# Performance work log

Hardware: AMD Instinct MI355X
Metric: run time of the kernel (lower is better)

Reference implementation:

```python
import jax, jax.numpy as jnp
import numpy as np

N, E, D = 50000, 800000, 128
NEG_SLOPE = 0.01  # torch LeakyReLU default


def _linear_params(key, fan_in, fan_out, bias=True):
    k1, k2 = jax.random.split(key)
    bound = 1.0 / np.sqrt(fan_in)
    W = jax.random.uniform(k1, (fan_in, fan_out), minval=-bound, maxval=bound, dtype=jnp.float32)
    if not bias:
        return W
    b = jax.random.uniform(k2, (fan_out,), minval=-bound, maxval=bound, dtype=jnp.float32)
    return W, b


def setup_inputs() -> dict:
    key = jax.random.key(0)
    ks = jax.random.split(key, 8)
    x = jax.random.normal(ks[0], (N, D), dtype=jnp.float32)
    edge_index = jax.random.randint(ks[1], (2, E), 0, N, dtype=jnp.int64)
    Wk, bk = _linear_params(ks[2], D, D)
    Wq, bq = _linear_params(ks[3], D, D)
    Wv, bv = _linear_params(ks[4], D, D)
    Wskip = _linear_params(ks[5], D, D, bias=False)  # lin_skip has bias=False
    b_conv = jnp.zeros((D,), dtype=jnp.float32)       # ResGatedGraphConv bias param
    Wlin, blin = _linear_params(ks[6], D, D)
    return {"x": x, "edge_index": edge_index, "Wk": Wk, "bk": bk, "Wq": Wq,
            "bq": bq, "Wv": Wv, "bv": bv, "Wskip": Wskip, "b_conv": b_conv,
            "Wlin": Wlin, "blin": blin}


def reference(x, edge_index, Wk, bk, Wq, bq, Wv, bv, Wskip, b_conv, Wlin, blin):
    src, dst = edge_index[0], edge_index[1]  # j -> i
    # dense projections on nodes (cheap), gather to edges (memory-bound)
    k = x @ Wk + bk          # [N, D] key of target
    q = x @ Wq + bq          # [N, D] query of source
    v = x @ Wv + bv          # [N, D] value of source
    gate = jax.nn.relu(k[dst] + q[src])      # act=ReLU() per module
    msg = gate * v[src]                       # [E, D]
    agg = jax.ops.segment_sum(msg, dst, num_segments=x.shape[0])  # scatter-add
    x1 = agg + x @ Wskip + b_conv            # root weight + bias
    x2 = jnp.where(x1 >= 0, x1, NEG_SLOPE * x1)  # LeakyReLU
    return x2 @ Wlin + blin
```

## Files before the change

### kernel.cpp

```cpp
#include <hip/hip_runtime.h>

#define DD 128

typedef __attribute__((ext_vector_type(8))) short bf16x8;
typedef __attribute__((ext_vector_type(4))) float f32x4;

__device__ inline unsigned short f2bf(float f) {
    unsigned int u = __float_as_uint(f);
    u += 0x7FFFu + ((u >> 16) & 1u);
    return (unsigned short)(u >> 16);
}
__device__ inline float bf2f(unsigned short s) {
    return __uint_as_float(((unsigned int)s) << 16);
}

template <typename T> __device__ inline T cvt(float f);
template <> __device__ inline float cvt<float>(float f) { return f; }
template <> __device__ inline unsigned short cvt<unsigned short>(float f) { return f2bf(f); }

template <typename T> __device__ inline float2 ld2(const T* p);
template <> __device__ inline float2 ld2<float>(const float* p) {
    return *reinterpret_cast<const float2*>(p);
}
template <> __device__ inline float2 ld2<unsigned short>(const unsigned short* p) {
    const ushort2 u = *reinterpret_cast<const ushort2*>(p);
    return make_float2(bf2f(u.x), bf2f(u.y));
}


__global__ __launch_bounds__(256) void split_w_kernel(
    const float* __restrict__ W0, const float* __restrict__ W1,
    const float* __restrict__ W2, const float* __restrict__ W3,
    const float* __restrict__ W4,
    unsigned short* __restrict__ whi,
    int* __restrict__ deg, int* __restrict__ cnt2, int* __restrict__ done,
    int N)
{
    const int gid = blockIdx.x * 256 + threadIdx.x;
    if (gid < N) { deg[gid] = 0; cnt2[gid] = 0; }
    if (gid == 0) *done = 0;

    const int idx = gid;
    if (idx >= 5 * 2048) return;
    const int mat  = idx >> 11;
    const int rem  = idx & 2047;
    const int ks   = rem >> 9;
    const int nt   = (rem >> 6) & 7;
    const int lane = rem & 63;
    const int lr = lane & 15, lg = lane >> 4;
    const float* __restrict__ W = mat == 0 ? W0 : mat == 1 ? W1 : mat == 2 ? W2
                                 : mat == 3 ? W3 : W4;
    const int n = nt * 16 + lr;
    bf16x8 h8;
#pragma unroll
    for (int r = 0; r < 8; ++r) {
        const int k = ks * 32 + lg * 8 + r;
        h8[r] = (short)f2bf(W[k * DD + n]);
    }
    *reinterpret_cast<bf16x8*>(&whi[(long)idx * 8]) = h8;
}

template <bool XFORM>
__device__ inline void stage_rows512(const float* __restrict__ src,
                                     const float* __restrict__ addv,
                                     int row0, int N, int t,
                                     unsigned short* __restrict__ ldsA)
{
    const int m  = t >> 3;
    const int gr = row0 + m;
#pragma unroll
    for (int j = 0; j < 2; ++j) {
        const int o = (t & 7) + j * 8;
        float v[8];
        if (gr < N) {
            const float4 a = *reinterpret_cast<const float4*>(&src[(long)gr * DD + o * 8]);
            const float4 b = *reinterpret_cast<const float4*>(&src[(long)gr * DD + o * 8 + 4]);
            v[0] = a.x; v[1] = a.y; v[2] = a.z; v[3] = a.w;
            v[4] = b.x; v[5] = b.y; v[6] = b.z; v[7] = b.w;
        } else {
#pragma unroll
            for (int e = 0; e < 8; ++e) v[e] = 0.f;
        }
        if (XFORM) {
#pragma unroll
            for (int e = 0; e < 8; ++e) {
                const float s = v[e] + addv[o * 8 + e];
                v[e] = s >= 0.f ? s : 0.01f * s;
            }
        }
        bf16x8 h8;
#pragma unroll
        for (int e = 0; e < 8; ++e) h8[e] = (short)f2bf(v[e]);
        const int rt   = m >> 4;
        const int ks   = o >> 2;
        const int lane = (m & 15) + (o & 3) * 16;
        const int base = ((rt * 4 + ks) * 64 + lane) * 8;
        *reinterpret_cast<bf16x8*>(&ldsA[base]) = h8;
    }
}

__global__ __launch_bounds__(512) void proj_mfma_kernel(
    const float* __restrict__ x,
    const unsigned short* __restrict__ whi,
    const float* __restrict__ bk, const float* __restrict__ bq,
    const float* __restrict__ bv,
    float* __restrict__ kbuf, unsigned short* __restrict__ qvpk,
    float* __restrict__ agg,
    const int* __restrict__ ei, int* __restrict__ deg,
    int projBlocks, int E, int N)
{
    __shared__ unsigned short ldsA[16 * 64 * 8];
    const int t = threadIdx.x;

    if (blockIdx.x >= projBlocks) {
        const int e = (blockIdx.x - projBlocks) * 512 + t;
        if (e < E) atomicAdd(&deg[ei[E + e]], 1);
        return;
    }

    const int row0 = blockIdx.x * 64;
    stage_rows512<false>(x, nullptr, row0, N, t, ldsA);
    __syncthreads();

    const int wv   = t >> 6;
    const int mat  = wv >> 1;
    const int cc   = wv & 1;
    const int lane = t & 63;
    const int lr = lane & 15;
    const int lg = lane >> 4;
    const float* bias = (mat == 0) ? bk : (mat == 1) ? bq : (mat == 2) ? bv : nullptr;

    f32x4 acc[4][4];
#pragma unroll
    for (int rt = 0; rt < 4; ++rt)
#pragma unroll
        for (int ct = 0; ct < 4; ++ct) acc[rt][ct] = (f32x4){0.f, 0.f, 0.f, 0.f};

#pragma unroll
    for (int ks = 0; ks < 4; ++ks) {
        bf16x8 A[4];
#pragma unroll
        for (int rt = 0; rt < 4; ++rt)
            A[rt] = *reinterpret_cast<const bf16x8*>(&ldsA[((rt * 4 + ks) * 64 + lane) * 8]);
#pragma unroll
        for (int ct = 0; ct < 4; ++ct) {
            const long fb = ((long)((mat * 4 + ks) * 8 + (cc * 4 + ct)) * 64 + lane) * 8;
            const bf16x8 B = *reinterpret_cast<const bf16x8*>(&whi[fb]);
#pragma unroll
            for (int rt = 0; rt < 4; ++rt)
                acc[rt][ct] = __builtin_amdgcn_mfma_f32_16x16x32_bf16(A[rt], B, acc[rt][ct], 0, 0, 0);
        }
    }

#pragma unroll
    for (int ct = 0; ct < 4; ++ct) {
        const int n_l = cc * 64 + ct * 16 + lr;
        const float bv_ = bias ? bias[n_l] : 0.f;
#pragma unroll
        for (int rt = 0; rt < 4; ++rt) {
#pragma unroll
            for (int r = 0; r < 4; ++r) {
                const int m = row0 + rt * 16 + lg * 4 + r;
                if (m < N) {
                    const float val = acc[rt][ct][r] + bv_;
                    if      (mat == 0) kbuf [(long)m * 128 + n_l]         = val;
                    else if (mat == 1) qvpk [(long)m * 256 + 2 * n_l]     = f2bf(val);
                    else if (mat == 2) qvpk [(long)m * 256 + 2 * n_l + 1] = f2bf(val);
                    else               agg  [(long)m * 128 + n_l]         = val;
                }
            }
        }
    }
}

__global__ __launch_bounds__(1024) void scanAB_kernel(
    const int* __restrict__ deg, int* __restrict__ off,
    int* __restrict__ bsum, int* __restrict__ done, int N, int nb)
{
    __shared__ int sm[1024];
    __shared__ int amLast;
    const int t = threadIdx.x;
    const int i = blockIdx.x * 1024 + t;
    const int v = (i < N) ? deg[i] : 0;
    int x = v;
    sm[t] = x;
    __syncthreads();
#pragma unroll
    for (int ofs = 1; ofs < 1024; ofs <<= 1) {
        const int y = (t >= ofs) ? sm[t - ofs] : 0;
        __syncthreads();
        x += y;
        sm[t] = x;
        __syncthreads();
    }
    if (i < N) off[i] = x - v;
    if (t == 1023) { bsum[blockIdx.x] = x; __threadfence(); }
    __syncthreads();
    if (t == 0) amLast = (atomicAdd(done, 1) == (int)gridDim.x - 1) ? 1 : 0;
    __syncthreads();
    if (!amLast) return;

    const int vb = (t < nb) ? atomicAdd(&bsum[t], 0) : 0;
    int xb = vb;
    sm[t] = xb;
    __syncthreads();
#pragma unroll
    for (int ofs = 1; ofs < 1024; ofs <<= 1) {
        const int y = (t >= ofs) ? sm[t - ofs] : 0;
        __syncthreads();
        xb += y;
        sm[t] = xb;
        __syncthreads();
    }
    if (t < nb) bsum[t] = xb - vb;
}

__global__ __launch_bounds__(256) void scatter2_kernel(
    const int* __restrict__ ei,
    const int* __restrict__ off, const int* __restrict__ bsum,
    int* __restrict__ cnt2, int* __restrict__ ssrc, int E)
{
    const int e = blockIdx.x * 256 + threadIdx.x;
    if (e >= E) return;
    const int s = ei[e];
    const int d = ei[E + e];
    const int pos = off[d] + bsum[d >> 10] + atomicAdd(&cnt2[d], 1);
    ssrc[pos] = s;
}

__global__ __launch_bounds__(512) void out_mfma_kernel(
    const float* agg, const float* __restrict__ bconv,
    const unsigned short* __restrict__ whi,
    const float* __restrict__ blin,
    float* out, int N)
{
    __shared__ unsigned short ldsA[16 * 64 * 8];
    const int t = threadIdx.x;
    const int row0 = blockIdx.x * 64;

    stage_rows512<true>(agg, bconv, row0, N, t, ldsA);
    __syncthreads();

    const int wv   = t >> 6;
    const int lane = t & 63;
    const int lr = lane & 15;
    const int lg = lane >> 4;

    f32x4 acc[4];
#pragma unroll
    for (int rt = 0; rt < 4; ++rt) acc[rt] = (f32x4){0.f, 0.f, 0.f, 0.f};

#pragma unroll
    for (int ks = 0; ks < 4; ++ks) {
        bf16x8 A[4];
#pragma unroll
        for (int rt = 0; rt < 4; ++rt)
            A[rt] = *reinterpret_cast<const bf16x8*>(&ldsA[((rt * 4 + ks) * 64 + lane) * 8]);
        const long fb = ((long)((16 + ks) * 8 + wv) * 64 + lane) * 8;
        const bf16x8 B = *reinterpret_cast<const bf16x8*>(&whi[fb]);
#pragma unroll
        for (int rt = 0; rt < 4; ++rt)
            acc[rt] = __builtin_amdgcn_mfma_f32_16x16x32_bf16(A[rt], B, acc[rt], 0, 0, 0);
    }

    const int n = wv * 16 + lr;
    const float bb = blin[n];
#pragma unroll
    for (int rt = 0; rt < 4; ++rt) {
#pragma unroll
        for (int r = 0; r < 4; ++r) {
            const int m = row0 + rt * 16 + lg * 4 + r;
            if (m < N) out[(long)m * 128 + n] = acc[rt][r] + bb;
        }
    }
}

__global__ __launch_bounds__(256) void gather_packed_kernel(
    const int* __restrict__ off, const int* __restrict__ bsum,
    const int* __restrict__ deg, const int* __restrict__ ssrc,
    const float* __restrict__ kbuf, const unsigned short* __restrict__ qvpk,
    float* __restrict__ agg, int N)
{
    const int n = blockIdx.x * 4 + (threadIdx.x >> 6);
    if (n >= N) return;
    const int lane = threadIdx.x & 63;

    const int dg = deg[n];
    if (dg == 0) return;
    const int s0 = off[n] + bsum[n >> 10];
    const int s1 = s0 + dg;

    const float2 k2 = *reinterpret_cast<const float2*>(&kbuf[(long)n * 128 + lane * 2]);
    float a0 = 0.f, a1 = 0.f, b0 = 0.f, b1 = 0.f;

    int e = s0;
    for (; e + 8 <= s1; e += 8) {
        int s[8];
#pragma unroll
        for (int j = 0; j < 8; ++j) s[j] = ssrc[e + j];
        ushort4 u[8];
#pragma unroll
        for (int j = 0; j < 8; ++j)
            u[j] = *reinterpret_cast<const ushort4*>(&qvpk[(long)s[j] * 256 + lane * 4]);
#pragma unroll
        for (int j = 0; j < 8; ++j) {
            const float q0 = bf2f(u[j].x), v0 = bf2f(u[j].y);
            const float q1 = bf2f(u[j].z), v1 = bf2f(u[j].w);
            if (j & 1) {
                b0 = fmaf(fmaxf(k2.x + q0, 0.f), v0, b0);
                b1 = fmaf(fmaxf(k2.y + q1, 0.f), v1, b1);
            } else {
                a0 = fmaf(fmaxf(k2.x + q0, 0.f), v0, a0);
                a1 = fmaf(fmaxf(k2.y + q1, 0.f), v1, a1);
            }
        }
    }
    for (; e < s1; ++e) {
        const int s = ssrc[e];
        const ushort4 u = *reinterpret_cast<const ushort4*>(&qvpk[(long)s * 256 + lane * 4]);
        a0 = fmaf(fmaxf(k2.x + bf2f(u.x), 0.f), bf2f(u.y), a0);
        a1 = fmaf(fmaxf(k2.y + bf2f(u.z), 0.f), bf2f(u.w), a1);
    }

    float2* ap = reinterpret_cast<float2*>(&agg[(long)n * 128 + lane * 2]);
    const float2 old = *ap;
    *ap = make_float2(old.x + a0 + b0, old.y + a1 + b1);
}

template <typename T>
__global__ __launch_bounds__(256) void proj_kernel(
    const float* __restrict__ x,
    const float* __restrict__ Wk, const float* __restrict__ bk,
    const float* __restrict__ Wq, const float* __restrict__ bq,
    const float* __restrict__ Wv, const float* __restrict__ bv,
    const float* __restrict__ Ws,
    T* __restrict__ kbuf, T* __restrict__ qvbuf, float* __restrict__ agg,
    int N)
{
    __shared__ float xt[32][DD];
    const int row0 = blockIdx.x * 32;
    const int t = threadIdx.x;

    for (int i = t; i < 32 * (DD / 4); i += 256) {
        const int r  = i >> 5;
        const int c4 = (i & 31) << 2;
        const int gr = row0 + r;
        float4 v = make_float4(0.f, 0.f, 0.f, 0.f);
        if (gr < N) v = *reinterpret_cast<const float4*>(&x[(long)gr * DD + c4]);
        *reinterpret_cast<float4*>(&xt[r][c4]) = v;
    }
    __syncthreads();

    const int c0 = t & 127;
    const int hi = t >> 7;
    const float* __restrict__ W0 = hi ? Wq : Wk;
    const float* __restrict__ W1 = hi ? Ws : Wv;
    const float b0 = hi ? bq[c0] : bk[c0];
    const float b1 = hi ? 0.f    : bv[c0];

    float acc0[32], acc1[32];
#pragma unroll
    for (int r = 0; r < 32; ++r) { acc0[r] = 0.f; acc1[r] = 0.f; }

    for (int k4 = 0; k4 < DD; k4 += 4) {
        const float w00 = W0[(k4 + 0) * DD + c0];
        const float w01 = W0[(k4 + 1) * DD + c0];
        const float w02 = W0[(k4 + 2) * DD + c0];
        const float w03 = W0[(k4 + 3) * DD + c0];
        const float w10 = W1[(k4 + 0) * DD + c0];
        const float w11 = W1[(k4 + 1) * DD + c0];
        const float w12 = W1[(k4 + 2) * DD + c0];
        const float w13 = W1[(k4 + 3) * DD + c0];
#pragma unroll
        for (int r = 0; r < 32; ++r) {
            const float4 xv = *reinterpret_cast<const float4*>(&xt[r][k4]);
            acc0[r] = fmaf(xv.x, w00, fmaf(xv.y, w01, fmaf(xv.z, w02, fmaf(xv.w, w03, acc0[r]))));
            acc1[r] = fmaf(xv.x, w10, fmaf(xv.y, w11, fmaf(xv.z, w12, fmaf(xv.w, w13, acc1[r]))));
        }
    }

#pragma unroll
    for (int r = 0; r < 32; ++r) {
        const long gr = row0 + r;
        if (gr < N) {
            if (hi == 0) {
                kbuf [gr * 128 + c0]       = cvt<T>(acc0[r] + b0);
                qvbuf[gr * 256 + 128 + c0] = cvt<T>(acc1[r] + b1);
            } else {
                qvbuf[gr * 256 + c0]       = cvt<T>(acc0[r] + b0);
                agg  [gr * 128 + c0]       = acc1[r];
            }
        }
    }
}

__global__ __launch_bounds__(256) void zero_kernel(int* __restrict__ p, int n) {
    const int i = blockIdx.x * 256 + threadIdx.x;
    if (i < n) p[i] = 0;
}

__global__ __launch_bounds__(256) void hist_kernel(
    const int* __restrict__ ei, int* __restrict__ deg, int E)
{
    const int e = blockIdx.x * 256 + threadIdx.x;
    if (e < E) atomicAdd(&deg[ei[E + e]], 1);
}

__global__ __launch_bounds__(1024) void scanA_kernel(
    const int* __restrict__ deg, int* __restrict__ off,
    int* __restrict__ bsum, int N)
{
    __shared__ int sm[1024];
    const int t = threadIdx.x;
    const int i = blockIdx.x * 1024 + t;
    const int v = (i < N) ? deg[i] : 0;
    int x = v;
    sm[t] = x;
    __syncthreads();
#pragma unroll
    for (int ofs = 1; ofs < 1024; ofs <<= 1) {
        const int y = (t >= ofs) ? sm[t - ofs] : 0;
        __syncthreads();
        x += y;
        sm[t] = x;
        __syncthreads();
    }
    if (i < N) off[i] = x - v;
    if (t == 1023) bsum[blockIdx.x] = x;
}

__global__ __launch_bounds__(1024) void scanB_kernel(int* __restrict__ bsum, int nb)
{
    __shared__ int sm[1024];
    const int t = threadIdx.x;
    const int v = (t < nb) ? bsum[t] : 0;
    int x = v;
    sm[t] = x;
    __syncthreads();
#pragma unroll
    for (int ofs = 1; ofs < 1024; ofs <<= 1) {
        const int y = (t >= ofs) ? sm[t - ofs] : 0;
        __syncthreads();
        x += y;
        sm[t] = x;
        __syncthreads();
    }
    if (t < nb) bsum[t] = x - v;
}

__global__ __launch_bounds__(256) void scanC_kernel(
    int* __restrict__ off, int* __restrict__ cursor,
    const int* __restrict__ bsum, int N)
{
    const int i = blockIdx.x * 256 + threadIdx.x;
    if (i < N) {
        const int o = off[i] + bsum[i >> 10];
        off[i]    = o;
        cursor[i] = o;
    }
}

__global__ __launch_bounds__(256) void scatter_kernel(
    const int* __restrict__ ei, int* __restrict__ cursor,
    int* __restrict__ ssrc, int E)
{
    const int e = blockIdx.x * 256 + threadIdx.x;
    if (e >= E) return;
    const int s = ei[e];
    const int d = ei[E + e];
    const int pos = atomicAdd(&cursor[d], 1);
    ssrc[pos] = s;
}

template <typename T>
__global__ __launch_bounds__(256) void gather_kernel(
    const int* __restrict__ off, const int* __restrict__ deg,
    const int* __restrict__ ssrc,
    const T* __restrict__ kbuf, const T* __restrict__ qvbuf,
    float* __restrict__ agg, int N)
{
    const int n = blockIdx.x * 4 + (threadIdx.x >> 6);
    if (n >= N) return;
    const int lane = threadIdx.x & 63;
    const int c = lane << 1;

    const int dg = deg[n];
    if (dg == 0) return;
    const int s0 = off[n];
    const int s1 = s0 + dg;

    const float2 k2 = ld2<T>(&kbuf[(long)n * 128 + c]);
    float a0 = 0.f, a1 = 0.f, b0 = 0.f, b1 = 0.f;

    int e = s0;
    for (; e + 4 <= s1; e += 4) {
        const long sa = ssrc[e + 0];
        const long sb = ssrc[e + 1];
        const long sc = ssrc[e + 2];
        const long sd = ssrc[e + 3];
        const float2 qa = ld2<T>(&qvbuf[sa * 256 + c]);
        const float2 va = ld2<T>(&qvbuf[sa * 256 + 128 + c]);
        const float2 qb = ld2<T>(&qvbuf[sb * 256 + c]);
        const float2 vb = ld2<T>(&qvbuf[sb * 256 + 128 + c]);
        const float2 qc = ld2<T>(&qvbuf[sc * 256 + c]);
        const float2 vc = ld2<T>(&qvbuf[sc * 256 + 128 + c]);
        const float2 qd = ld2<T>(&qvbuf[sd * 256 + c]);
        const float2 vd = ld2<T>(&qvbuf[sd * 256 + 128 + c]);
        a0 = fmaf(fmaxf(k2.x + qa.x, 0.f), va.x, a0);
        a1 = fmaf(fmaxf(k2.y + qa.y, 0.f), va.y, a1);
        b0 = fmaf(fmaxf(k2.x + qb.x, 0.f), vb.x, b0);
        b1 = fmaf(fmaxf(k2.y + qb.y, 0.f), vb.y, b1);
        a0 = fmaf(fmaxf(k2.x + qc.x, 0.f), vc.x, a0);
        a1 = fmaf(fmaxf(k2.y + qc.y, 0.f), vc.y, a1);
        b0 = fmaf(fmaxf(k2.x + qd.x, 0.f), vd.x, b0);
        b1 = fmaf(fmaxf(k2.y + qd.y, 0.f), vd.y, b1);
    }
    for (; e < s1; ++e) {
        const long s = ssrc[e];
        const float2 q = ld2<T>(&qvbuf[s * 256 + c]);
        const float2 v = ld2<T>(&qvbuf[s * 256 + 128 + c]);
        a0 = fmaf(fmaxf(k2.x + q.x, 0.f), v.x, a0);
        a1 = fmaf(fmaxf(k2.y + q.y, 0.f), v.y, a1);
    }

    float2* ap = reinterpret_cast<float2*>(&agg[(long)n * 128 + c]);
    const float2 old = *ap;
    *ap = make_float2(old.x + a0 + b0, old.y + a1 + b1);
}

template <typename T>
__global__ __launch_bounds__(256) void edge_kernel(
    const int* __restrict__ ei,
    const T* __restrict__ kbuf, const T* __restrict__ qvbuf,
    float* __restrict__ agg, int E)
{
    const int g = (blockIdx.x << 3) + (threadIdx.x >> 5);
    if (g >= E) return;
    const int lane = threadIdx.x & 31;
    const long src = (long)ei[g];
    const long dst = (long)ei[E + g];
    const int c = lane << 2;

    float kd[4], qs[4], vs[4];
    if constexpr (sizeof(T) == 4) {
        const float4 a = *reinterpret_cast<const float4*>(&kbuf[dst * 128 + c]);
        const float4 b = *reinterpret_cast<const float4*>(&qvbuf[src * 256 + c]);
        const float4 d = *reinterpret_cast<const float4*>(&qvbuf[src * 256 + 128 + c]);
        kd[0] = a.x; kd[1] = a.y; kd[2] = a.z; kd[3] = a.w;
        qs[0] = b.x; qs[1] = b.y; qs[2] = b.z; qs[3] = b.w;
        vs[0] = d.x; vs[1] = d.y; vs[2] = d.z; vs[3] = d.w;
    } else {
        const ushort4 a = *reinterpret_cast<const ushort4*>(&kbuf[dst * 128 + c]);
        const ushort4 b = *reinterpret_cast<const ushort4*>(&qvbuf[src * 256 + c]);
        const ushort4 d = *reinterpret_cast<const ushort4*>(&qvbuf[src * 256 + 128 + c]);
        kd[0] = bf2f(a.x); kd[1] = bf2f(a.y); kd[2] = bf2f(a.z); kd[3] = bf2f(a.w);
        qs[0] = bf2f(b.x); qs[1] = bf2f(b.y); qs[2] = bf2f(b.z); qs[3] = bf2f(b.w);
        vs[0] = bf2f(d.x); vs[1] = bf2f(d.y); vs[2] = bf2f(d.z); vs[3] = bf2f(d.w);
    }

    float* p = agg + dst * 128 + c;
#pragma unroll
    for (int j = 0; j < 4; ++j) {
        const float m = fmaxf(kd[j] + qs[j], 0.f) * vs[j];
        unsafeAtomicAdd(p + j, m);
    }
}

__global__ __launch_bounds__(64) void out_kernel(
    const float* agg, const float* __restrict__ bconv,
    const float* __restrict__ Wlin, const float* __restrict__ blin,
    float* out, int N)
{
    __shared__ float xt[32][DD];
    const int row0 = blockIdx.x * 32;
    const int t = threadIdx.x;

    for (int i = t; i < 32 * (DD / 4); i += 64) {
        const int r  = i >> 5;
        const int c4 = (i & 31) << 2;
        const int gr = row0 + r;
        float4 a = make_float4(0.f, 0.f, 0.f, 0.f);
        if (gr < N) a = *reinterpret_cast<const float4*>(&agg[(long)gr * DD + c4]);
        const float4 b = *reinterpret_cast<const float4*>(&bconv[c4]);
        float4 v;
        const float x0 = a.x + b.x; v.x = x0 >= 0.f ? x0 : 0.01f * x0;
        const float x1 = a.y + b.y; v.y = x1 >= 0.f ? x1 : 0.01f * x1;
        const float x2 = a.z + b.z; v.z = x2 >= 0.f ? x2 : 0.01f * x2;
        const float x3 = a.w + b.w; v.w = x3 >= 0.f ? x3 : 0.01f * x3;
        *reinterpret_cast<float4*>(&xt[r][c4]) = v;
    }
    __syncthreads();

    const int c0 = t;
    const int c1 = t + 64;
    float acc0[32], acc1[32];
#pragma unroll
    for (int r = 0; r < 32; ++r) { acc0[r] = 0.f; acc1[r] = 0.f; }

    for (int k4 = 0; k4 < DD; k4 += 4) {
        const float w00 = Wlin[(k4 + 0) * DD + c0];
        const float w01 = Wlin[(k4 + 1) * DD + c0];
        const float w02 = Wlin[(k4 + 2) * DD + c0];
        const float w03 = Wlin[(k4 + 3) * DD + c0];
        const float w10 = Wlin[(k4 + 0) * DD + c1];
        const float w11 = Wlin[(k4 + 1) * DD + c1];
        const float w12 = Wlin[(k4 + 2) * DD + c1];
        const float w13 = Wlin[(k4 + 3) * DD + c1];
#pragma unroll
        for (int r = 0; r < 32; ++r) {
            const float4 xv = *reinterpret_cast<const float4*>(&xt[r][k4]);
            acc0[r] = fmaf(xv.x, w00, fmaf(xv.y, w01, fmaf(xv.z, w02, fmaf(xv.w, w03, acc0[r]))));
            acc1[r] = fmaf(xv.x, w10, fmaf(xv.y, w11, fmaf(xv.z, w12, fmaf(xv.w, w13, acc1[r]))));
        }
    }

    const float bb0 = blin[c0];
    const float bb1 = blin[c1];
#pragma unroll
    for (int r = 0; r < 32; ++r) {
        const long gr = row0 + r;
        if (gr < N) {
            out[gr * DD + c0] = acc0[r] + bb0;
            out[gr * DD + c1] = acc1[r] + bb1;
        }
    }
}

extern "C" void kernel_launch(void* const* d_in, const int* in_sizes, int n_in,
                              void* d_out, int out_size, void* d_ws, size_t ws_size,
                              hipStream_t stream)
{
    const float* x     = (const float*)d_in[0];
    const int*   ei    = (const int*)d_in[1];
    const float* Wk    = (const float*)d_in[2];
    const float* bk    = (const float*)d_in[3];
    const float* Wq    = (const float*)d_in[4];
    const float* bq    = (const float*)d_in[5];
    const float* Wv    = (const float*)d_in[6];
    const float* bv    = (const float*)d_in[7];
    const float* Ws    = (const float*)d_in[8];
    const float* bconv = (const float*)d_in[9];
    const float* Wlin  = (const float*)d_in[10];
    const float* blin  = (const float*)d_in[11];

    const int N = in_sizes[0] / DD;
    const int E = in_sizes[1] / 2;

    float* aggf = (float*)d_out;
    const int nblk    = (N + 31) / 32;
    const int mblk    = (N + 63) / 64;
    const int eblk1   = (E + 255) / 256;
    const int nblk1   = (N + 255) / 256;
    const int gblk    = (N + 3) / 4;
    const int nchunks = (N + 1023) / 1024;
    const int hblk    = (E + 511) / 512;

    const int bsum_pad = (nchunks + 255) & ~255;

    size_t csrF_ints = (size_t)3 * N + bsum_pad + 256 + E;
    csrF_ints = (csrF_ints + 3) & ~(size_t)3;
    const size_t csrF_bytes = csrF_ints * sizeof(int);

    size_t csrO_ints = (size_t)3 * N + bsum_pad + E;
    csrO_ints = (csrO_ints + 3) & ~(size_t)3;
    const size_t csrO_bytes = csrO_ints * sizeof(int);

    const size_t projPK   = (size_t)N * (128 * sizeof(float) + 256 * sizeof(unsigned short));
    const size_t projF32  = (size_t)N * 384 * sizeof(float);
    const size_t projBF16 = (size_t)N * 384 * sizeof(unsigned short);
    const size_t wsplit   = (size_t)5 * 2048 * 8 * sizeof(unsigned short);

    if (ws_size >= csrF_bytes + projPK + wsplit) {
        int* deg  = (int*)d_ws;
        int* off  = deg + N;
        int* cnt2 = off + N;
        int* bsum = cnt2 + N;
        int* done = bsum + bsum_pad;
        int* ssrc = done + 256;
        float* kbuf = (float*)((char*)d_ws + csrF_bytes);
        unsigned short* qvpk = (unsigned short*)(kbuf + (size_t)N * 128);
        unsigned short* whi  = qvpk + (size_t)N * 256;

        const int swblk = (N + 255) / 256;
        split_w_kernel<<<swblk, 256, 0, stream>>>(Wk, Wq, Wv, Ws, Wlin, whi,
                                                  deg, cnt2, done, N);
        proj_mfma_kernel<<<mblk + hblk, 512, 0, stream>>>(x, whi, bk, bq, bv,
                                                          kbuf, qvpk, aggf,
                                                          ei, deg, mblk, E, N);
        scanAB_kernel<<<nchunks, 1024, 0, stream>>>(deg, off, bsum, done, N, nchunks);
        scatter2_kernel<<<eblk1, 256, 0, stream>>>(ei, off, bsum, cnt2, ssrc, E);
        gather_packed_kernel<<<gblk, 256, 0, stream>>>(off, bsum, deg, ssrc, kbuf, qvpk, aggf, N);
        out_mfma_kernel<<<mblk, 512, 0, stream>>>(aggf, bconv, whi, blin, (float*)d_out, N);
    } else if (ws_size >= csrO_bytes + projF32) {
        int* deg    = (int*)d_ws;
        int* off    = deg + N;
        int* cursor = off + N;
        int* bsum   = cursor + N;
        int* ssrc   = bsum + bsum_pad;
        float* kbuf  = (float*)((char*)d_ws + csrO_bytes);
        float* qvbuf = kbuf + (size_t)N * 128;

        proj_kernel<float><<<nblk, 256, 0, stream>>>(x, Wk, bk, Wq, bq, Wv, bv, Ws,
                                                     kbuf, qvbuf, aggf, N);
        zero_kernel<<<nblk1, 256, 0, stream>>>(deg, N);
        hist_kernel<<<eblk1, 256, 0, stream>>>(ei, deg, E);
        scanA_kernel<<<nchunks, 1024, 0, stream>>>(deg, off, bsum, N);
        scanB_kernel<<<1, 1024, 0, stream>>>(bsum, nchunks);
        scanC_kernel<<<nblk1, 256, 0, stream>>>(off, cursor, bsum, N);
        scatter_kernel<<<eblk1, 256, 0, stream>>>(ei, cursor, ssrc, E);
        gather_kernel<float><<<gblk, 256, 0, stream>>>(off, deg, ssrc, kbuf, qvbuf, aggf, N);
        out_kernel<<<nblk, 64, 0, stream>>>(aggf, bconv, Wlin, blin, (float*)d_out, N);
    } else if (ws_size >= csrO_bytes + projBF16) {
        int* deg    = (int*)d_ws;
        int* off    = deg + N;
        int* cursor = off + N;
        int* bsum   = cursor + N;
        int* ssrc   = bsum + bsum_pad;
        unsigned short* kbuf  = (unsigned short*)((char*)d_ws + csrO_bytes);
        unsigned short* qvbuf = kbuf + (size_t)N * 128;

        proj_kernel<unsigned short><<<nblk, 256, 0, stream>>>(x, Wk, bk, Wq, bq, Wv, bv, Ws,
                                                              kbuf, qvbuf, aggf, N);
        zero_kernel<<<nblk1, 256, 0, stream>>>(deg, N);
        hist_kernel<<<eblk1, 256, 0, stream>>>(ei, deg, E);
        scanA_kernel<<<nchunks, 1024, 0, stream>>>(deg, off, bsum, N);
        scanB_kernel<<<1, 1024, 0, stream>>>(bsum, nchunks);
        scanC_kernel<<<nblk1, 256, 0, stream>>>(off, cursor, bsum, N);
        scatter_kernel<<<eblk1, 256, 0, stream>>>(ei, cursor, ssrc, E);
        gather_kernel<unsigned short><<<gblk, 256, 0, stream>>>(off, deg, ssrc, kbuf, qvbuf, aggf, N);
        out_kernel<<<nblk, 64, 0, stream>>>(aggf, bconv, Wlin, blin, (float*)d_out, N);
    } else if (ws_size >= projBF16) {
        unsigned short* kbuf  = (unsigned short*)d_ws;
        unsigned short* qvbuf = kbuf + (size_t)N * 128;
        const int eblk8 = (E + 7) / 8;
        proj_kernel<unsigned short><<<nblk, 256, 0, stream>>>(x, Wk, bk, Wq, bq, Wv, bv, Ws,
                                                              kbuf, qvbuf, aggf, N);
        edge_kernel<unsigned short><<<eblk8, 256, 0, stream>>>(ei, kbuf, qvbuf, aggf, E);
        out_kernel<<<nblk, 64, 0, stream>>>(aggf, bconv, Wlin, blin, (float*)d_out, N);
    } else {
        hipMemsetAsync(d_out, 0, (size_t)out_size * sizeof(float), stream);
        return;
    }
}
```

Measured before the change: 229.0 us.

## Fuse edge gather with output projection and store keys as bf16

Merges the per-node gather/aggregate kernel into the final MFMA projection kernel. Each wave aggregates 8 nodes, applies bias and LeakyReLU, and writes bf16 rows straight into the LDS tile, so the fp32 aggregate no longer makes a round trip through global memory and one launch is dropped. The key projection is now stored as bf16 instead of fp32, halving its footprint and read traffic at some cost in precision. The risk is load imbalance: each block now serializes 8 variable-degree nodes per wave before the MFMA stage, with fewer, larger blocks than the old gather launch.

```diff
diff --git a/kernel.cpp b/kernel.cpp
--- a/kernel.cpp
+++ b/kernel.cpp
@@ -60,9 +60,7 @@
     *reinterpret_cast<bf16x8*>(&whi[(long)idx * 8]) = h8;
 }
 
-template <bool XFORM>
 __device__ inline void stage_rows512(const float* __restrict__ src,
-                                     const float* __restrict__ addv,
                                      int row0, int N, int t,
                                      unsigned short* __restrict__ ldsA)
 {
@@ -81,13 +79,6 @@
 #pragma unroll
             for (int e = 0; e < 8; ++e) v[e] = 0.f;
         }
-        if (XFORM) {
-#pragma unroll
-            for (int e = 0; e < 8; ++e) {
-                const float s = v[e] + addv[o * 8 + e];
-                v[e] = s >= 0.f ? s : 0.01f * s;
-            }
-        }
         bf16x8 h8;
 #pragma unroll
         for (int e = 0; e < 8; ++e) h8[e] = (short)f2bf(v[e]);
@@ -104,7 +95,7 @@
     const unsigned short* __restrict__ whi,
     const float* __restrict__ bk, const float* __restrict__ bq,
     const float* __restrict__ bv,
-    float* __restrict__ kbuf, unsigned short* __restrict__ qvpk,
+    unsigned short* __restrict__ kbuf, unsigned short* __restrict__ qvpk,
     float* __restrict__ agg,
     const int* __restrict__ ei, int* __restrict__ deg,
     int projBlocks, int E, int N)
@@ -119,7 +110,7 @@
     }
 
     const int row0 = blockIdx.x * 64;
-    stage_rows512<false>(x, nullptr, row0, N, t, ldsA);
+    stage_rows512(x, row0, N, t, ldsA);
     __syncthreads();
 
     const int wv   = t >> 6;
@@ -163,7 +154,7 @@
                 const int m = row0 + rt * 16 + lg * 4 + r;
                 if (m < N) {
                     const float val = acc[rt][ct][r] + bv_;
-                    if      (mat == 0) kbuf [(long)m * 128 + n_l]         = val;
+                    if      (mat == 0) kbuf [(long)m * 128 + n_l]         = f2bf(val);
                     else if (mat == 1) qvpk [(long)m * 256 + 2 * n_l]     = f2bf(val);
                     else if (mat == 2) qvpk [(long)m * 256 + 2 * n_l + 1] = f2bf(val);
                     else               agg  [(long)m * 128 + n_l]         = val;
@@ -228,28 +219,87 @@
     ssrc[pos] = s;
 }
 
-__global__ __launch_bounds__(512) void out_mfma_kernel(
+__global__ __launch_bounds__(512) void gather_out_kernel(
+    const int* __restrict__ off, const int* __restrict__ bsum,
+    const int* __restrict__ deg, const int* __restrict__ ssrc,
+    const unsigned short* __restrict__ kbuf, const unsigned short* __restrict__ qvpk,
     const float* agg, const float* __restrict__ bconv,
-    const unsigned short* __restrict__ whi,
-    const float* __restrict__ blin,
+    const unsigned short* __restrict__ whi, const float* __restrict__ blin,
     float* out, int N)
 {
     __shared__ unsigned short ldsA[16 * 64 * 8];
     const int t = threadIdx.x;
     const int row0 = blockIdx.x * 64;
-
-    stage_rows512<true>(agg, bconv, row0, N, t, ldsA);
-    __syncthreads();
-
     const int wv   = t >> 6;
     const int lane = t & 63;
+
+    const float bc0 = bconv[lane * 2];
+    const float bc1 = bconv[lane * 2 + 1];
+
+    const int ksl   = lane >> 4;
+    const int lgrp  = (lane >> 2) & 3;
+    const int eoff  = (2 * lane) & 7;
+
+#pragma unroll 1
+    for (int j = 0; j < 8; ++j) {
+        const int n = row0 + wv * 8 + j;
+        float a0 = 0.f, a1 = 0.f, b0 = 0.f, b1 = 0.f;
+        if (n < N) {
+            const float2 sk = *reinterpret_cast<const float2*>(&agg[(long)n * 128 + lane * 2]);
+            const ushort2 ku = *reinterpret_cast<const ushort2*>(&kbuf[(long)n * 128 + lane * 2]);
+            const float k0 = bf2f(ku.x), k1 = bf2f(ku.y);
+            a0 = sk.x; a1 = sk.y;
+
+            const int dg = deg[n];
+            const int s0 = off[n] + bsum[n >> 10];
+            const int s1 = s0 + dg;
+            int e = s0;
+            for (; e + 8 <= s1; e += 8) {
+                int s[8];
+#pragma unroll
+                for (int u = 0; u < 8; ++u) s[u] = ssrc[e + u];
+                ushort4 q[8];
+#pragma unroll
+                for (int u = 0; u < 8; ++u)
+                    q[u] = *reinterpret_cast<const ushort4*>(&qvpk[(long)s[u] * 256 + lane * 4]);
+#pragma unroll
+                for (int u = 0; u < 8; ++u) {
+                    const float q0 = bf2f(q[u].x), v0 = bf2f(q[u].y);
+                    const float q1 = bf2f(q[u].z), v1 = bf2f(q[u].w);
+                    if (u & 1) {
+                        b0 = fmaf(fmaxf(k0 + q0, 0.f), v0, b0);
+                        b1 = fmaf(fmaxf(k1 + q1, 0.f), v1, b1);
+                    } else {
+                        a0 = fmaf(fmaxf(k0 + q0, 0.f), v0, a0);
+                        a1 = fmaf(fmaxf(k1 + q1, 0.f), v1, a1);
+                    }
+                }
+            }
+            for (; e < s1; ++e) {
+                const int s = ssrc[e];
+                const ushort4 q = *reinterpret_cast<const ushort4*>(&qvpk[(long)s * 256 + lane * 4]);
+                a0 = fmaf(fmaxf(k0 + bf2f(q.x), 0.f), bf2f(q.y), a0);
+                a1 = fmaf(fmaxf(k1 + bf2f(q.z), 0.f), bf2f(q.w), a1);
+            }
+        }
+        float x0 = a0 + b0 + bc0; x0 = x0 >= 0.f ? x0 : 0.01f * x0;
+        float x1 = a1 + b1 + bc1; x1 = x1 >= 0.f ? x1 : 0.01f * x1;
+        const int m  = wv * 8 + j;
+        const int rt = m >> 4;
+        const int ln2 = (m & 15) + 16 * lgrp;
+        ushort2 hh;
+        hh.x = f2bf(x0);
+        hh.y = f2bf(x1);
+        *reinterpret_cast<ushort2*>(&ldsA[((rt * 4 + ksl) * 64 + ln2) * 8 + eoff]) = hh;
+    }
+    __syncthreads();
+
+    f32x4 acc[4];
+#pragma unroll
+    for (int rt = 0; rt < 4; ++rt) acc[rt] = (f32x4){0.f, 0.f, 0.f, 0.f};
+
     const int lr = lane & 15;
     const int lg = lane >> 4;
-
-    f32x4 acc[4];
-#pragma unroll
-    for (int rt = 0; rt < 4; ++rt) acc[rt] = (f32x4){0.f, 0.f, 0.f, 0.f};
-
 #pragma unroll
     for (int ks = 0; ks < 4; ++ks) {
         bf16x8 A[4];
@@ -273,58 +323,6 @@
             if (m < N) out[(long)m * 128 + n] = acc[rt][r] + bb;
         }
     }
-}
-
-__global__ __launch_bounds__(256) void gather_packed_kernel(
-    const int* __restrict__ off, const int* __restrict__ bsum,
-    const int* __restrict__ deg, const int* __restrict__ ssrc,
-    const float* __restrict__ kbuf, const unsigned short* __restrict__ qvpk,
-    float* __restrict__ agg, int N)
-{
-    const int n = blockIdx.x * 4 + (threadIdx.x >> 6);
-    if (n >= N) return;
-    const int lane = threadIdx.x & 63;
-
-    const int dg = deg[n];
-    if (dg == 0) return;
-    const int s0 = off[n] + bsum[n >> 10];
-    const int s1 = s0 + dg;
-
-    const float2 k2 = *reinterpret_cast<const float2*>(&kbuf[(long)n * 128 + lane * 2]);
-    float a0 = 0.f, a1 = 0.f, b0 = 0.f, b1 = 0.f;
-
-    int e = s0;
-    for (; e + 8 <= s1; e += 8) {
-        int s[8];
-#pragma unroll
-        for (int j = 0; j < 8; ++j) s[j] = ssrc[e + j];
-        ushort4 u[8];
-#pragma unroll
-        for (int j = 0; j < 8; ++j)
-            u[j] = *reinterpret_cast<const ushort4*>(&qvpk[(long)s[j] * 256 + lane * 4]);
-#pragma unroll
-        for (int j = 0; j < 8; ++j) {
-            const float q0 = bf2f(u[j].x), v0 = bf2f(u[j].y);
-            const float q1 = bf2f(u[j].z), v1 = bf2f(u[j].w);
-            if (j & 1) {
-                b0 = fmaf(fmaxf(k2.x + q0, 0.f), v0, b0);
-                b1 = fmaf(fmaxf(k2.y + q1, 0.f), v1, b1);
-            } else {
-                a0 = fmaf(fmaxf(k2.x + q0, 0.f), v0, a0);
-                a1 = fmaf(fmaxf(k2.y + q1, 0.f), v1, a1);
-            }
-        }
-    }
-    for (; e < s1; ++e) {
-        const int s = ssrc[e];
-        const ushort4 u = *reinterpret_cast<const ushort4*>(&qvpk[(long)s * 256 + lane * 4]);
-        a0 = fmaf(fmaxf(k2.x + bf2f(u.x), 0.f), bf2f(u.y), a0);
-        a1 = fmaf(fmaxf(k2.y + bf2f(u.z), 0.f), bf2f(u.w), a1);
-    }
-
-    float2* ap = reinterpret_cast<float2*>(&agg[(long)n * 128 + lane * 2]);
-    const float2 old = *ap;
-    *ap = make_float2(old.x + a0 + b0, old.y + a1 + b1);
 }
 
 template <typename T>
@@ -665,7 +663,7 @@
     csrO_ints = (csrO_ints + 3) & ~(size_t)3;
     const size_t csrO_bytes = csrO_ints * sizeof(int);
 
-    const size_t projPK   = (size_t)N * (128 * sizeof(float) + 256 * sizeof(unsigned short));
+    const size_t projPK   = (size_t)N * (128 + 256) * sizeof(unsigned short);
     const size_t projF32  = (size_t)N * 384 * sizeof(float);
     const size_t projBF16 = (size_t)N * 384 * sizeof(unsigned short);
     const size_t wsplit   = (size_t)5 * 2048 * 8 * sizeof(unsigned short);
@@ -677,8 +675,8 @@
         int* bsum = cnt2 + N;
         int* done = bsum + bsum_pad;
         int* ssrc = done + 256;
-        float* kbuf = (float*)((char*)d_ws + csrF_bytes);
-        unsigned short* qvpk = (unsigned short*)(kbuf + (size_t)N * 128);
+        unsigned short* kbuf = (unsigned short*)((char*)d_ws + csrF_bytes);
+        unsigned short* qvpk = kbuf + (size_t)N * 128;
         unsigned short* whi  = qvpk + (size_t)N * 256;
 
         const int swblk = (N + 255) / 256;
@@ -689,8 +687,9 @@
                                                           ei, deg, mblk, E, N);
         scanAB_kernel<<<nchunks, 1024, 0, stream>>>(deg, off, bsum, done, N, nchunks);
         scatter2_kernel<<<eblk1, 256, 0, stream>>>(ei, off, bsum, cnt2, ssrc, E);
-        gather_packed_kernel<<<gblk, 256, 0, stream>>>(off, bsum, deg, ssrc, kbuf, qvpk, aggf, N);
-        out_mfma_kernel<<<mblk, 512, 0, stream>>>(aggf, bconv, whi, blin, (float*)d_out, N);
+        gather_out_kernel<<<mblk, 512, 0, stream>>>(off, bsum, deg, ssrc,
+                                                    kbuf, qvpk, aggf, bconv,
+                                                    whi, blin, (float*)d_out, N);
     } else if (ws_size >= csrO_bytes + projF32) {
         int* deg    = (int*)d_ws;
         int* off    = deg + N;
```

Result: slower. 252.2 us, median of 2 (+10.1%).
